# Performance work log

Measured on AMD Instinct MI355X. Metric: run time of the kernel, lower is better.

## Reference

```python
import jax, jax.numpy as jnp
import numpy as np

N_NODES = 100000


def setup_inputs() -> dict:
    key = jax.random.key(0)
    k1, k2, k3, k4, k5, k6 = jax.random.split(key, 6)
    n_edges = 1600000
    X = jax.random.normal(k1, (N_NODES, 256), dtype=jnp.float32)
    edge_row = jax.random.randint(k2, (n_edges,), 0, N_NODES, dtype=jnp.int64)
    edge_col = jax.random.randint(k3, (n_edges,), 0, N_NODES, dtype=jnp.int64)
    edge_val = jax.random.uniform(k4, (n_edges,), dtype=jnp.float32)
    W = jax.random.normal(k5, (128, 256), dtype=jnp.float32) * 0.05
    b = jax.random.normal(k6, (128,), dtype=jnp.float32) * 0.05
    return {"X": X, "edge_row": edge_row, "edge_col": edge_col,
            "edge_val": edge_val, "W": W, "b": b}


def reference(X, edge_row, edge_col, edge_val, W, b):
    # Dense projection: H = X @ W^T + b  -> [N, out_dim]
    H = jnp.einsum('ni,oi->no', X, W) + b
    # SpMM: out[r] = sum_e A[r, c_e] * H[c_e] over edges with row r
    msgs = edge_val[:, None] * H[edge_col]          # [E, out_dim]
    out = jax.ops.segment_sum(msgs, edge_row, num_segments=N_NODES)
    return out
```

## Files before the change

### kernel.cpp

```cpp
#include <hip/hip_runtime.h>
#include <hip/hip_bf16.h>

#define NNODES 100000
#define NEDGES 1600000
#define KDIM 256
#define ODIM 128
#define NB_SCAN 98
#define EDGE_CAP 1900032
#define ESTRIDE 400000
#define GEMM_BLOCKS 1563
#define RANK_BLOCKS 1563

typedef __attribute__((ext_vector_type(8))) short short8;
typedef __attribute__((ext_vector_type(4))) float floatx4;

static __device__ __forceinline__ short f2bf(float f) {
  union { float f; unsigned u; } x; x.f = f;
  unsigned r = (x.u + 0x7fffu + ((x.u >> 16) & 1u)) >> 16;
  return (short)r;
}

__global__ void conv_w_kernel(const float* __restrict__ W, short* __restrict__ Wb) {
  int i = blockIdx.x * 256 + threadIdx.x;
  if (i < ODIM * KDIM) Wb[i] = f2bf(W[i]);
}

__global__ void scan1_kernel(const int* __restrict__ counts, int* __restrict__ chunkExcl,
                             int* __restrict__ blockSums) {
  __shared__ int s[256];
  int t = threadIdx.x;
  int base = blockIdx.x * 1024 + t * 4;
  int v[4];
#pragma unroll
  for (int j = 0; j < 4; j++) {
    int idx = base + j;
    v[j] = (idx < NNODES) ? ((counts[idx] + 3) & ~3) : 0;
  }
  int sum = v[0] + v[1] + v[2] + v[3];
  s[t] = sum;
  __syncthreads();
  for (int o = 1; o < 256; o <<= 1) {
    int add = (t >= o) ? s[t - o] : 0;
    __syncthreads();
    s[t] += add;
    __syncthreads();
  }
  int run = s[t] - sum;
#pragma unroll
  for (int j = 0; j < 4; j++) {
    int idx = base + j;
    if (idx < NNODES) chunkExcl[idx] = run;
    run += v[j];
  }
  if (t == 255) blockSums[blockIdx.x] = s[255];
}

__global__ void scan2_kernel(const int* __restrict__ blockSums, int* __restrict__ blockBase,
                             int* __restrict__ offsets) {
  __shared__ int s[128];
  int t = threadIdx.x;
  int v = (t < NB_SCAN) ? blockSums[t] : 0;
  s[t] = v;
  __syncthreads();
  for (int o = 1; o < 128; o <<= 1) {
    int add = (t >= o) ? s[t - o] : 0;
    __syncthreads();
    s[t] += add;
    __syncthreads();
  }
  if (t < NB_SCAN) blockBase[t] = s[t] - v;
  if (t == 127) offsets[NNODES] = s[127];
}

__global__ void scan3_kernel(const int* __restrict__ chunkExcl, const int* __restrict__ blockBase,
                             int* __restrict__ offsets) {
  int i = blockIdx.x * 256 + threadIdx.x;
  if (i < NNODES) offsets[i] = chunkExcl[i] + blockBase[i >> 10];
}

__global__ void place_kernel(const int* __restrict__ rows, const int* __restrict__ cols,
                             const float* __restrict__ vals,
                             const unsigned short* __restrict__ rank,
                             const int* __restrict__ offsets, int2* __restrict__ edges) {
  int i = blockIdx.x * 256 + threadIdx.x;
#pragma unroll
  for (int j = 0; j < 4; j++) {
    int e = i + j * ESTRIDE;
    if (e < NEDGES) {
      int r = rows[e];
      int p = offsets[r] + (int)rank[e];
      int2 rec;
      rec.x = cols[e];
      rec.y = __float_as_int(vals[e]);
      edges[p] = rec;
    }
  }
}

__global__ __launch_bounds__(256) void gemm_rank_kernel(
    const float* __restrict__ X, const short* __restrict__ Wb,
    const float* __restrict__ bias, unsigned short* __restrict__ H,
    const int* __restrict__ rows, int* __restrict__ counts,
    unsigned short* __restrict__ rank) {
  if (blockIdx.x >= GEMM_BLOCKS) {
    int i = (blockIdx.x - GEMM_BLOCKS) * 256 + threadIdx.x;
#pragma unroll
    for (int j = 0; j < 4; j++) {
      int e = i + j * ESTRIDE;
      if (e < NEDGES) {
        int r = rows[e];
        rank[e] = (unsigned short)atomicAdd(&counts[r], 1);
      }
    }
    return;
  }
  const int lane = threadIdx.x & 63;
  const int wave = threadIdx.x >> 6;
  const int l16 = lane & 15;
  const int quad = lane >> 4;
  const int rowBase = blockIdx.x * 64 + wave * 16;
  const int arow = rowBase + l16;
  const bool inb = arow < NNODES;
  const float4 zf4 = {0.f, 0.f, 0.f, 0.f};
  const float4* xp = (const float4*)(X + (size_t)(inb ? arow : 0) * KDIM);

  float4 xv[16];
#pragma unroll
  for (int k0 = 0; k0 < 8; k0++) {
    xv[2 * k0] = inb ? xp[quad * 2 + k0 * 8] : zf4;
    xv[2 * k0 + 1] = inb ? xp[quad * 2 + k0 * 8 + 1] : zf4;
  }

  floatx4 acc[8];
#pragma unroll
  for (int t = 0; t < 8; t++) acc[t] = (floatx4){0.f, 0.f, 0.f, 0.f};

#pragma unroll
  for (int k0 = 0; k0 < 8; k0++) {
    const float4 c0 = xv[2 * k0];
    const float4 c1 = xv[2 * k0 + 1];
    short8 a;
    a[0] = f2bf(c0.x); a[1] = f2bf(c0.y); a[2] = f2bf(c0.z); a[3] = f2bf(c0.w);
    a[4] = f2bf(c1.x); a[5] = f2bf(c1.y); a[6] = f2bf(c1.z); a[7] = f2bf(c1.w);
    const short* bp = Wb + k0 * 32 + quad * 8;
#pragma unroll
    for (int t = 0; t < 8; t++) {
      short8 b = *(const short8*)(bp + (size_t)(t * 16 + l16) * KDIM);
      acc[t] = __builtin_amdgcn_mfma_f32_16x16x32_bf16(a, b, acc[t], 0, 0, 0);
    }
  }

#pragma unroll
  for (int t = 0; t < 8; t++) {
    const int col = t * 16 + l16;
    const float bv = bias[col];
#pragma unroll
    for (int r = 0; r < 4; r++) {
      const int row = rowBase + quad * 4 + r;
      if (row < NNODES) H[(size_t)row * ODIM + col] = (unsigned short)f2bf(acc[t][r] + bv);
    }
  }
}

__global__ __launch_bounds__(256) void spmm_kernel(const int* __restrict__ offsets,
                                                   const int2* __restrict__ edges,
                                                   const unsigned* __restrict__ H2,
                                                   float* __restrict__ out) {
  const int lane = threadIdx.x & 63;
  const int wid = blockIdx.x * 4 + (threadIdx.x >> 6);
  const int r0 = wid * 2;
  const int r1 = r0 + 1;
  if (r0 >= NNODES) return;
  const int s0 = offsets[r0];
  const int s1 = offsets[r1];
  const int e1 = offsets[r1 + 1];
  const int len0 = s1 - s0;
  const int len1 = e1 - s1;
  const int2* p0 = edges + s0;
  const int2* p1 = edges + s1;
  float ax0 = 0.f, ay0 = 0.f, ax1 = 0.f, ay1 = 0.f;
  const int it = len0 > len1 ? len0 : len1;
#define EDGE_ACC(px, py, ax, ay)                              \
  {                                                           \
    const unsigned h = H2[(size_t)(px) * 64 + lane];          \
    const float v = __int_as_float(py);                       \
    ax += v * __uint_as_float(h << 16);                       \
    ay += v * __uint_as_float(h & 0xffff0000u);               \
  }
  for (int i = 0; i < it; i += 4) {
    if (i < len0) {
      const int4 a01 = *(const int4*)(p0 + i);
      const int4 a23 = *(const int4*)(p0 + i + 2);
      EDGE_ACC(a01.x, a01.y, ax0, ay0)
      EDGE_ACC(a01.z, a01.w, ax0, ay0)
      EDGE_ACC(a23.x, a23.y, ax0, ay0)
      EDGE_ACC(a23.z, a23.w, ax0, ay0)
    }
    if (i < len1) {
      const int4 b01 = *(const int4*)(p1 + i);
      const int4 b23 = *(const int4*)(p1 + i + 2);
      EDGE_ACC(b01.x, b01.y, ax1, ay1)
      EDGE_ACC(b01.z, b01.w, ax1, ay1)
      EDGE_ACC(b23.x, b23.y, ax1, ay1)
      EDGE_ACC(b23.z, b23.w, ax1, ay1)
    }
  }
#undef EDGE_ACC
  float2 o0, o1;
  o0.x = ax0; o0.y = ay0;
  o1.x = ax1; o1.y = ay1;
  ((float2*)out)[(size_t)r0 * 64 + lane] = o0;
  ((float2*)out)[(size_t)r1 * 64 + lane] = o1;
}

extern "C" void kernel_launch(void* const* d_in, const int* in_sizes, int n_in,
                              void* d_out, int out_size, void* d_ws, size_t ws_size,
                              hipStream_t stream) {
  const float* X = (const float*)d_in[0];
  const int* erow = (const int*)d_in[1];
  const int* ecol = (const int*)d_in[2];
  const float* eval = (const float*)d_in[3];
  const float* W = (const float*)d_in[4];
  const float* bias = (const float*)d_in[5];
  float* out = (float*)d_out;

  char* ws = (char*)d_ws;
  size_t off = 0;
  auto alloc = [&](size_t bytes) -> char* {
    char* p = ws + off;
    off += (bytes + 255) & ~(size_t)255;
    return p;
  };
  unsigned short* Hb = (unsigned short*)alloc((size_t)NNODES * ODIM * 2);
  short* Wb = (short*)alloc((size_t)ODIM * KDIM * 2);
  int* counts = (int*)alloc((size_t)NNODES * 4);
  int* chunkExcl = (int*)alloc((size_t)NNODES * 4);
  int* offsets = (int*)alloc((size_t)(NNODES + 1) * 4);
  int* blockSums = (int*)alloc((size_t)NB_SCAN * 4);
  int* blockBase = (int*)alloc((size_t)NB_SCAN * 4);
  unsigned short* rank = (unsigned short*)alloc((size_t)NEDGES * 2);
  int2* edges = (int2*)alloc((size_t)EDGE_CAP * 8);

  hipMemsetAsync(counts, 0, (size_t)NNODES * 4, stream);
  hipMemsetAsync(edges, 0, (size_t)EDGE_CAP * 8, stream);
  conv_w_kernel<<<(ODIM * KDIM + 255) / 256, 256, 0, stream>>>(W, Wb);
  gemm_rank_kernel<<<GEMM_BLOCKS + RANK_BLOCKS, 256, 0, stream>>>(X, Wb, bias, Hb,
                                                                 erow, counts, rank);
  scan1_kernel<<<NB_SCAN, 256, 0, stream>>>(counts, chunkExcl, blockSums);
  scan2_kernel<<<1, 128, 0, stream>>>(blockSums, blockBase, offsets);
  scan3_kernel<<<(NNODES + 255) / 256, 256, 0, stream>>>(chunkExcl, blockBase, offsets);
  place_kernel<<<(ESTRIDE + 255) / 256, 256, 0, stream>>>(erow, ecol, eval, rank, offsets, edges);
  spmm_kernel<<<(NNODES / 2 + 3) / 4, 256, 0, stream>>>(offsets, edges, (const unsigned*)Hb, out);
}
```

Before: 435.0 us.

## Restructure GEMM to stage X tiles in LDS via global_load_lds with register-resident W

The GEMM part now runs 512-thread blocks in which 8 waves split the 128 output columns into two halves. Each wave keeps its W fragments in registers. Tiles of X are streamed into double-buffered, XOR-swizzled shared memory with asynchronous global_load_lds, and a barrier separates each K step. The aim is coalesced X loads and less repeated strided W traffic from global memory. The cost is a barrier per K step and higher register pressure from the 32 short8 fragments. Rank blocks are resized to 512 threads, and redundant bounds checks in place and rank are dropped.

```diff
diff --git a/kernel.cpp b/kernel.cpp
--- a/kernel.cpp
+++ b/kernel.cpp
@@ -9,10 +9,12 @@
 #define EDGE_CAP 1900032
 #define ESTRIDE 400000
 #define GEMM_BLOCKS 1563
-#define RANK_BLOCKS 1563
+#define RANK_BLOCKS 782
 
 typedef __attribute__((ext_vector_type(8))) short short8;
 typedef __attribute__((ext_vector_type(4))) float floatx4;
+typedef const __attribute__((address_space(1))) unsigned gas_u32;
+typedef __attribute__((address_space(3))) unsigned lds_u32;
 
 static __device__ __forceinline__ short f2bf(float f) {
   union { float f; unsigned u; } x; x.f = f;
@@ -83,80 +85,93 @@
                              const unsigned short* __restrict__ rank,
                              const int* __restrict__ offsets, int2* __restrict__ edges) {
   int i = blockIdx.x * 256 + threadIdx.x;
+  if (i >= ESTRIDE) return;
 #pragma unroll
   for (int j = 0; j < 4; j++) {
     int e = i + j * ESTRIDE;
-    if (e < NEDGES) {
-      int r = rows[e];
-      int p = offsets[r] + (int)rank[e];
-      int2 rec;
-      rec.x = cols[e];
-      rec.y = __float_as_int(vals[e]);
-      edges[p] = rec;
-    }
-  }
-}
-
-__global__ __launch_bounds__(256) void gemm_rank_kernel(
+    int r = rows[e];
+    int p = offsets[r] + (int)rank[e];
+    int2 rec;
+    rec.x = cols[e];
+    rec.y = __float_as_int(vals[e]);
+    edges[p] = rec;
+  }
+}
+
+__global__ __launch_bounds__(512) void gemm_rank_kernel(
     const float* __restrict__ X, const short* __restrict__ Wb,
     const float* __restrict__ bias, unsigned short* __restrict__ H,
     const int* __restrict__ rows, int* __restrict__ counts,
     unsigned short* __restrict__ rank) {
+  __shared__ float xs[2][2048];
+
   if (blockIdx.x >= GEMM_BLOCKS) {
-    int i = (blockIdx.x - GEMM_BLOCKS) * 256 + threadIdx.x;
+    int i = (blockIdx.x - GEMM_BLOCKS) * 512 + threadIdx.x;
+    if (i >= ESTRIDE) return;
 #pragma unroll
     for (int j = 0; j < 4; j++) {
       int e = i + j * ESTRIDE;
-      if (e < NEDGES) {
-        int r = rows[e];
-        rank[e] = (unsigned short)atomicAdd(&counts[r], 1);
-      }
+      int r = rows[e];
+      rank[e] = (unsigned short)atomicAdd(&counts[r], 1);
     }
     return;
   }
-  const int lane = threadIdx.x & 63;
-  const int wave = threadIdx.x >> 6;
+
+  const int tid = threadIdx.x;
+  const int w = tid >> 6;
+  const int lane = tid & 63;
   const int l16 = lane & 15;
   const int quad = lane >> 4;
-  const int rowBase = blockIdx.x * 64 + wave * 16;
-  const int arow = rowBase + l16;
-  const bool inb = arow < NNODES;
-  const float4 zf4 = {0.f, 0.f, 0.f, 0.f};
-  const float4* xp = (const float4*)(X + (size_t)(inb ? arow : 0) * KDIM);
-
-  float4 xv[16];
-#pragma unroll
-  for (int k0 = 0; k0 < 8; k0++) {
-    xv[2 * k0] = inb ? xp[quad * 2 + k0 * 8] : zf4;
-    xv[2 * k0 + 1] = inb ? xp[quad * 2 + k0 * 8 + 1] : zf4;
-  }
-
-  floatx4 acc[8];
-#pragma unroll
-  for (int t = 0; t < 8; t++) acc[t] = (floatx4){0.f, 0.f, 0.f, 0.f};
-
-#pragma unroll
-  for (int k0 = 0; k0 < 8; k0++) {
-    const float4 c0 = xv[2 * k0];
-    const float4 c1 = xv[2 * k0 + 1];
+  const int wr = w & 3;
+  const int wc = w >> 2;
+  const int rowBase = blockIdx.x * 64;
+
+  short8 bfrag[4][8];
+#pragma unroll
+  for (int t = 0; t < 4; t++) {
+    const short* bp = Wb + (size_t)(wc * 64 + t * 16 + l16) * KDIM + quad * 8;
+#pragma unroll
+    for (int k = 0; k < 8; k++) bfrag[t][k] = *(const short8*)(bp + k * 32);
+  }
+
+  const int rl = lane >> 3;
+  const int ch = lane & 7;
+  int grow = rowBase + w * 8 + rl;
+  if (grow >= NNODES) grow = NNODES - 1;
+  const float* gsrc = X + (size_t)grow * KDIM + ((ch ^ rl) << 2);
+
+  floatx4 acc[4];
+#pragma unroll
+  for (int t = 0; t < 4; t++) acc[t] = (floatx4){0.f, 0.f, 0.f, 0.f};
+
+  __builtin_amdgcn_global_load_lds((gas_u32*)gsrc, (lds_u32*)&xs[0][w * 256], 16, 0, 0);
+  __syncthreads();
+
+#pragma unroll
+  for (int k = 0; k < 8; k++) {
+    if (k < 7) {
+      __builtin_amdgcn_global_load_lds((gas_u32*)(gsrc + (k + 1) * 32),
+                                       (lds_u32*)&xs[(k + 1) & 1][w * 256], 16, 0, 0);
+    }
+    const float* base = &xs[k & 1][(wr * 16 + l16) * 32];
+    const float4 c0 = *(const float4*)(base + (((2 * quad) ^ (l16 & 7)) << 2));
+    const float4 c1 = *(const float4*)(base + (((2 * quad + 1) ^ (l16 & 7)) << 2));
     short8 a;
     a[0] = f2bf(c0.x); a[1] = f2bf(c0.y); a[2] = f2bf(c0.z); a[3] = f2bf(c0.w);
     a[4] = f2bf(c1.x); a[5] = f2bf(c1.y); a[6] = f2bf(c1.z); a[7] = f2bf(c1.w);
-    const short* bp = Wb + k0 * 32 + quad * 8;
-#pragma unroll
-    for (int t = 0; t < 8; t++) {
-      short8 b = *(const short8*)(bp + (size_t)(t * 16 + l16) * KDIM);
-      acc[t] = __builtin_amdgcn_mfma_f32_16x16x32_bf16(a, b, acc[t], 0, 0, 0);
-    }
-  }
-
-#pragma unroll
-  for (int t = 0; t < 8; t++) {
-    const int col = t * 16 + l16;
+#pragma unroll
+    for (int t = 0; t < 4; t++)
+      acc[t] = __builtin_amdgcn_mfma_f32_16x16x32_bf16(a, bfrag[t][k], acc[t], 0, 0, 0);
+    __syncthreads();
+  }
+
+#pragma unroll
+  for (int t = 0; t < 4; t++) {
+    const int col = wc * 64 + t * 16 + l16;
     const float bv = bias[col];
 #pragma unroll
     for (int r = 0; r < 4; r++) {
-      const int row = rowBase + quad * 4 + r;
+      const int row = rowBase + wr * 16 + quad * 4 + r;
       if (row < NNODES) H[(size_t)row * ODIM + col] = (unsigned short)f2bf(acc[t][r] + bv);
     }
   }
@@ -244,8 +259,8 @@
   hipMemsetAsync(counts, 0, (size_t)NNODES * 4, stream);
   hipMemsetAsync(edges, 0, (size_t)EDGE_CAP * 8, stream);
   conv_w_kernel<<<(ODIM * KDIM + 255) / 256, 256, 0, stream>>>(W, Wb);
-  gemm_rank_kernel<<<GEMM_BLOCKS + RANK_BLOCKS, 256, 0, stream>>>(X, Wb, bias, Hb,
-                                                                 erow, counts, rank);
+  gemm_rank_kernel<<<GEMM_BLOCKS + RANK_BLOCKS, 512, 0, stream>>>(X, Wb, bias, Hb,
+                                                                  erow, counts, rank);
   scan1_kernel<<<NB_SCAN, 256, 0, stream>>>(counts, chunkExcl, blockSums);
   scan2_kernel<<<1, 128, 0, stream>>>(blockSums, blockBase, offsets);
   scan3_kernel<<<(NNODES + 255) / 256, 256, 0, stream>>>(chunkExcl, blockBase, offsets);
```

Result: faster. 425.6 us (-2.2%).
